# Performance work log

Measured on AMD Instinct MI355X. Metric: run time of the kernel, lower is better.

## Reference

```python
import jax, jax.numpy as jnp
import numpy as np

N, F, H, R, B, L, C, E, NB = 8192, 512, 256, 16, 32, 256, 7, 262144, 30
D = F + H


def setup_inputs() -> dict:
    ks = jax.random.split(jax.random.key(0), 16)
    g = lambda k, shape, fan: jax.random.normal(k, shape, jnp.float32) / np.sqrt(fan)
    return {
        "x": jax.random.normal(ks[0], (N, F), jnp.float32),
        "edge_index": jax.random.randint(ks[1], (2, E), 0, N),
        "edge_norm": jax.random.uniform(ks[2], (E,), jnp.float32),
        "edge_type": jax.random.randint(ks[3], (E,), 0, R),
        "seq_lengths": jnp.full((B,), L, dtype=jnp.int32),
        "umask": jnp.ones((B, L), jnp.float32),
        "nodal_attn": 1,
        "avec": 0,
        "basis": g(ks[4], (NB, F, H), F),
        "comp": g(ks[5], (R, NB), NB),
        "root1": g(ks[6], (F, H), F),
        "bias1": jnp.zeros((H,), jnp.float32),
        "w_rel": g(ks[7], (H, H), H),
        "b_rel": jnp.zeros((H,), jnp.float32),
        "w_root": g(ks[8], (H, H), H),
        "w_att": g(ks[9], (D, D), D),
        "b_att": jnp.zeros((D,), jnp.float32),
        "w_lin": g(ks[10], (D, H), D),
        "b_lin": jnp.zeros((H,), jnp.float32),
        "w_fc": g(ks[11], (H, C), H),
        "b_fc": jnp.zeros((C,), jnp.float32),
    }


def reference(x, edge_index, edge_norm, edge_type, seq_lengths, umask,
              nodal_attn, avec, basis, comp, root1, bias1, w_rel, b_rel,
              w_root, w_att, b_att, w_lin, b_lin, w_fc, b_fc):
    n = x.shape[0]
    r = comp.shape[0]
    src, dst = edge_index[0], edge_index[1]
    # ---- RGCNConv (num_bases basis decomposition, mean aggregation per relation, root + bias)
    W = jnp.einsum('rb,bfh->rfh', comp, basis)             # [R,F,H]
    xw = jnp.einsum('nf,rfh->nrh', x, W)                   # [N,R,H]
    msg = xw[src, edge_type]                               # [E,H] gather per edge
    seg = dst * r + edge_type                              # per (node, relation) segment
    cnt = jax.ops.segment_sum(jnp.ones((msg.shape[0],), msg.dtype), seg, num_segments=n * r)
    msg = msg / jnp.maximum(cnt[seg], 1.0)[:, None]
    out1 = jax.ops.segment_sum(msg, dst, num_segments=n) + x @ root1 + bias1
    # ---- GraphConv (add aggregation): W_rel * sum_j h_j + b_rel + W_root * h_i
    agg2 = jax.ops.segment_sum(out1[src], dst, num_segments=n)
    out2 = agg2 @ w_rel + b_rel + out1 @ w_root
    emotions = jnp.concatenate([x, out2], axis=-1)          # [N, F+H]
    if int(nodal_attn):
        seq = np.asarray(seq_lengths)                       # static conversation lengths
        starts = np.concatenate([[0], np.cumsum(seq)[:-1]])
        lmax = int(seq.max())
        rows = [jnp.pad(jax.lax.dynamic_slice_in_dim(emotions, int(s), int(l)),
                        ((0, lmax - int(l)), (0, 0)))
                for s, l in zip(starts, seq)]
        M = jnp.stack(rows, 0).transpose(1, 0, 2)           # [L, B, D]
        mask = umask                                        # [B, L]
        # MatchingAttention 'general2', vectorized over all timesteps t
        X = M @ w_att + b_att                               # transform(x_t) for every t: [L,B,D]
        Mm = M * mask.T[:, :, None]                         # mask memory over seq dim
        scores = jnp.einsum('tbd,sbd->tbs', X, Mm) * mask[None]
        a = jax.nn.softmax(jnp.tanh(scores), axis=-1) * mask[None]
        a = a / jnp.sum(a, axis=-1, keepdims=True)
        att = jnp.einsum('tbs,sbd->tbd', a, M)              # [L,B,D]
        hidden = jax.nn.relu(att @ w_lin + b_lin)
    else:
        hidden = jax.nn.relu(emotions @ w_lin + b_lin)
    # dropout is identity in eval mode
    logits = hidden @ w_fc + b_fc
    if int(avec):
        return logits
    return jax.nn.log_softmax(logits, axis=1)  # faithful: torch uses dim=1
```

## Files before the change

kernel.cpp:

```cpp
#include <hip/hip_runtime.h>
#include <hip/hip_bf16.h>

#define NN 8192
#define FF 512
#define HH 256
#define RR 16
#define BB 32
#define LL 256
#define CC 7
#define EE 262144
#define NBASE 30
#define DD 768

constexpr int FLAG_BIAS = 1, FLAG_RELU = 4, FLAG_TANH = 8,
              FLAG_SPLITOUT = 16, FLAG_TAILOUT = 32;

typedef __attribute__((ext_vector_type(8))) short bf16x8;
typedef __attribute__((ext_vector_type(4))) float f32x4;

__global__ __launch_bounds__(256) void detect_dtype(const unsigned short* __restrict__ xs,
                                                    int* __restrict__ flag) {
  __shared__ int red[256];
  int cnt = 0;
  for (int i = threadIdx.x * 2; i < 8192; i += 512) {
    unsigned short u = xs[i];
    int e = (u >> 7) & 0xFF;
    if (e >= 0xC0) cnt++;
  }
  red[threadIdx.x] = cnt;
  __syncthreads();
  for (int s = 128; s > 0; s >>= 1) {
    if (threadIdx.x < s) red[threadIdx.x] += red[threadIdx.x + s];
    __syncthreads();
  }
  if (threadIdx.x == 0) flag[0] = (red[0] > 16) ? 1 : 0;
}

struct ConvSeg {
  const void* src;
  float* dst;
  __hip_bfloat16* hi;
  __hip_bfloat16* lo;
  int n;
  int zero;
};
struct ConvTable {
  ConvSeg seg[12];
  int count;
  long total;
};

__global__ __launch_bounds__(256) void conv_all(ConvTable t, const int* __restrict__ flag) {
  const int fp32 = flag[0];
  for (long i = (long)blockIdx.x * 256 + threadIdx.x; i < t.total;
       i += (long)gridDim.x * 256) {
    long off = i;
    int s = 0;
    while (off >= t.seg[s].n) { off -= t.seg[s].n; s++; }
    const ConvSeg& sg = t.seg[s];
    float v = 0.f;
    if (!sg.zero)
      v = fp32 ? ((const float*)sg.src)[off]
               : __bfloat162float(((const __hip_bfloat16*)sg.src)[off]);
    if (sg.dst) sg.dst[off] = v;
    if (sg.hi) {
      __hip_bfloat16 h = __float2bfloat16(v);
      sg.hi[off] = h;
      sg.lo[off] = __float2bfloat16(v - __bfloat162float(h));
    }
  }
}

struct TSeg {
  const void* src;
  __hip_bfloat16* hi;
  __hip_bfloat16* lo;
  int R, C, ld, off;
};
struct TTable {
  TSeg seg[6];
  int count;
  long total;
};

__global__ __launch_bounds__(256) void split_t_all(TTable t, const int* __restrict__ flag) {
  const int fp32 = flag[0];
  for (long i = (long)blockIdx.x * 256 + threadIdx.x; i < t.total;
       i += (long)gridDim.x * 256) {
    long off = i;
    int s = 0;
    while (off >= (long)t.seg[s].R * t.seg[s].C) { off -= (long)t.seg[s].R * t.seg[s].C; s++; }
    const TSeg& sg = t.seg[s];
    int r = (int)(off % sg.R), c = (int)(off / sg.R);
    float v = fp32 ? ((const float*)sg.src)[(long)r * sg.C + c]
                   : __bfloat162float(((const __hip_bfloat16*)sg.src)[(long)r * sg.C + c]);
    __hip_bfloat16 h = __float2bfloat16(v);
    long d = (long)c * sg.ld + sg.off + r;
    sg.hi[d] = h;
    sg.lo[d] = __float2bfloat16(v - __bfloat162float(h));
  }
}

__global__ __launch_bounds__(256) void copy_xsplit(
    const __hip_bfloat16* __restrict__ xh, const __hip_bfloat16* __restrict__ xl,
    __hip_bfloat16* __restrict__ eh, __hip_bfloat16* __restrict__ el) {
  int idx = blockIdx.x * 256 + threadIdx.x;
  int n = idx >> 9, f = idx & 511;
  long d = (long)n * DD + f;
  eh[d] = xh[idx];
  el[d] = xl[idx];
}

__global__ __launch_bounds__(256) void transpose_emw(
    const __hip_bfloat16* __restrict__ hi_src, const __hip_bfloat16* __restrict__ lo_src,
    __hip_bfloat16* __restrict__ hi_dst, __hip_bfloat16* __restrict__ lo_dst) {
  __shared__ __hip_bfloat16 t[32][33];
  const int zz = blockIdx.z;
  const __hip_bfloat16* src = (zz < 32) ? hi_src : lo_src;
  __hip_bfloat16* dst = (zz < 32) ? hi_dst : lo_dst;
  const long b = zz & 31;
  const int d0 = blockIdx.x * 32, s0 = blockIdx.y * 32;
  const int c = threadIdx.x & 31, rw = threadIdx.x >> 5;
  const __hip_bfloat16* sp = src + b * (LL * 256);
  __hip_bfloat16* dp = dst + b * (LL * 256);
#pragma unroll
  for (int i = 0; i < 4; ++i)
    t[rw + i * 8][c] = sp[(long)(s0 + rw + i * 8) * 256 + d0 + c];
  __syncthreads();
#pragma unroll
  for (int i = 0; i < 4; ++i)
    dp[(long)(d0 + rw + i * 8) * 256 + s0 + c] = t[c][rw + i * 8];
}

__global__ __launch_bounds__(256) void wt_gemm(
    const float* __restrict__ basis, const float* __restrict__ comp,
    float* __restrict__ wt_nat) {
  __shared__ float cs[RR * NBASE];
  int tid = threadIdx.x;
  for (int i = tid; i < RR * NBASE; i += 256) cs[i] = comp[i];
  __syncthreads();
  long col = (long)blockIdx.x * 256 + tid;
  float acc[RR] = {};
  for (int b = 0; b < NBASE; ++b) {
    float v = basis[(long)b * 131072 + col];
#pragma unroll
    for (int r = 0; r < RR; ++r) acc[r] += cs[r * NBASE + b] * v;
  }
#pragma unroll
  for (int r = 0; r < RR; ++r) wt_nat[(long)r * 131072 + col] = acc[r];
}

__global__ __launch_bounds__(256) void wt_transpose(
    const float* __restrict__ wt_nat,
    __hip_bfloat16* __restrict__ hi, __hip_bfloat16* __restrict__ lo) {
  __shared__ float t[32][33];
  const int r = blockIdx.z;
  const int f0 = blockIdx.y * 32, h0 = blockIdx.x * 32;
  const int c = threadIdx.x & 31, rw = threadIdx.x >> 5;
  const float* src = wt_nat + ((long)r * 512 + f0) * 256 + h0;
#pragma unroll
  for (int i = 0; i < 4; ++i)
    t[rw + i * 8][c] = src[(long)(rw + i * 8) * 256 + c];
  __syncthreads();
#pragma unroll
  for (int i = 0; i < 4; ++i) {
    int hh = rw + i * 8;
    float v = t[c][hh];
    long orow = (long)(r * 256 + h0 + hh) * 512 + f0 + c;
    __hip_bfloat16 hv = __float2bfloat16(v);
    hi[orow] = hv;
    lo[orow] = __float2bfloat16(v - __bfloat162float(hv));
  }
}

__device__ __forceinline__ void gload_lds16(const void* g, void* l) {
  __builtin_amdgcn_global_load_lds(
      (const __attribute__((address_space(1))) unsigned int*)g,
      (__attribute__((address_space(3))) unsigned int*)l, 16, 0, 0);
}

__global__ __launch_bounds__(256, 3) void mfma_dual(
    const __hip_bfloat16* __restrict__ A, const __hip_bfloat16* __restrict__ Alo,
    const __hip_bfloat16* __restrict__ Bt, const __hip_bfloat16* __restrict__ Btlo,
    const float* __restrict__ bias, float* __restrict__ C, float* __restrict__ Ct,
    __hip_bfloat16* __restrict__ Chi, __hip_bfloat16* __restrict__ Clo,
    int K, int ldc, long sA, long sB, long sC, int flags) {
  __shared__ __hip_bfloat16 Ah[128 * 32];
  __shared__ __hip_bfloat16 Bh[128 * 32];
  __shared__ __hip_bfloat16 Al[128 * 32];
  __shared__ __hip_bfloat16 Bl[128 * 32];
  const int tid = threadIdx.x;
  const int w = tid >> 6, lane = tid & 63;
  const long z = blockIdx.z;
  const long row0 = (long)blockIdx.y * 128, col0 = (long)blockIdx.x * 128;
  const int wm = w & 1, wn = w >> 1;
  const int srow0 = (w * 128 + lane) >> 2;
  const int srow1 = (w * 128 + 64 + lane) >> 2;
  const int kch = (lane & 3) * 8;
  const int fr = lane & 15, q = lane >> 4;
  const bool hasAlo = (Alo != nullptr);
  const __hip_bfloat16* Az = A + z * sA;
  const __hip_bfloat16* Alz = hasAlo ? (Alo + z * sA) : nullptr;
  const __hip_bfloat16* Bz = Bt + z * sB;
  const __hip_bfloat16* Blz = Btlo + z * sB;
  const long aoff0 = (row0 + srow0) * K + kch, aoff1 = (row0 + srow1) * K + kch;
  const long boff0 = (col0 + srow0) * K + kch, boff1 = (col0 + srow1) * K + kch;
  f32x4 acc[4][4] = {};
  for (int k0 = 0; k0 < K; k0 += 32) {
    gload_lds16(Az + aoff0 + k0, Ah + w * 1024);
    gload_lds16(Az + aoff1 + k0, Ah + w * 1024 + 512);
    gload_lds16(Bz + boff0 + k0, Bh + w * 1024);
    gload_lds16(Bz + boff1 + k0, Bh + w * 1024 + 512);
    gload_lds16(Blz + boff0 + k0, Bl + w * 1024);
    gload_lds16(Blz + boff1 + k0, Bl + w * 1024 + 512);
    if (hasAlo) {
      gload_lds16(Alz + aoff0 + k0, Al + w * 1024);
      gload_lds16(Alz + aoff1 + k0, Al + w * 1024 + 512);
    }
    __syncthreads();
    bf16x8 ah[4], bh[4], bl[4];
#pragma unroll
    for (int i = 0; i < 4; ++i) {
      ah[i] = *(const bf16x8*)&Ah[(wm * 64 + i * 16 + fr) * 32 + q * 8];
      bh[i] = *(const bf16x8*)&Bh[(wn * 64 + i * 16 + fr) * 32 + q * 8];
      bl[i] = *(const bf16x8*)&Bl[(wn * 64 + i * 16 + fr) * 32 + q * 8];
    }
#pragma unroll
    for (int i = 0; i < 4; ++i)
#pragma unroll
      for (int j = 0; j < 4; ++j) {
        acc[i][j] = __builtin_amdgcn_mfma_f32_16x16x32_bf16(ah[i], bh[j], acc[i][j], 0, 0, 0);
        acc[i][j] = __builtin_amdgcn_mfma_f32_16x16x32_bf16(ah[i], bl[j], acc[i][j], 0, 0, 0);
      }
    if (hasAlo) {
      bf16x8 al[4];
#pragma unroll
      for (int i = 0; i < 4; ++i)
        al[i] = *(const bf16x8*)&Al[(wm * 64 + i * 16 + fr) * 32 + q * 8];
#pragma unroll
      for (int i = 0; i < 4; ++i)
#pragma unroll
        for (int j = 0; j < 4; ++j)
          acc[i][j] = __builtin_amdgcn_mfma_f32_16x16x32_bf16(al[i], bh[j], acc[i][j], 0, 0, 0);
    }
    __syncthreads();
  }
  const int cr = (lane >> 4) * 4, cc = lane & 15;
  float* Cz = C ? (C + z * sC) : nullptr;
  __hip_bfloat16* Chz = Chi ? (Chi + z * sC) : nullptr;
  __hip_bfloat16* Clz = Clo ? (Clo + z * sC) : nullptr;
#pragma unroll
  for (int i = 0; i < 4; ++i) {
    long rbase = row0 + wm * 64 + i * 16 + cr;
#pragma unroll
    for (int j = 0; j < 4; ++j) {
      long col = col0 + wn * 64 + j * 16 + cc;
      float bv = (flags & FLAG_BIAS) ? bias[col] : 0.f;
#pragma unroll
      for (int r = 0; r < 4; ++r) {
        float v = acc[i][j][r] + bv;
        if (flags & FLAG_RELU) v = fmaxf(v, 0.f);
        if (flags & FLAG_TANH) v = tanhf(v);
        if (flags & FLAG_SPLITOUT) {
          long off = (rbase + r) * ldc + col;
          __hip_bfloat16 hv = __float2bfloat16(v);
          Chz[off] = hv;
          Clz[off] = __float2bfloat16(v - __bfloat162float(hv));
        } else if ((flags & FLAG_TAILOUT) && col >= 4096) {
          Ct[(rbase + r) * 256 + (col - 4096)] = v;
        } else {
          Cz[(rbase + r) * ldc + col] = v;
        }
      }
    }
  }
}

__global__ __launch_bounds__(256) void count_edges(
    const int* __restrict__ ei, const int* __restrict__ et, float* __restrict__ cnt) {
  int e = blockIdx.x * 256 + threadIdx.x;
  if (e < EE) atomicAdd(&cnt[ei[EE + e] * RR + et[e]], 1.0f);
}

__global__ __launch_bounds__(256) void scan_rowptr(
    const float* __restrict__ cntf, int* __restrict__ rowptr, int* __restrict__ fill) {
  __shared__ int part[256];
  int tid = threadIdx.x;
  int base = tid * 32;
  int local[32];
  int s = 0;
  for (int i = 0; i < 32; ++i) {
    local[i] = s;
    const float* c = &cntf[(base + i) * RR];
    int d = 0;
#pragma unroll
    for (int r = 0; r < RR; ++r) d += (int)c[r];
    s += d;
  }
  part[tid] = s;
  __syncthreads();
  for (int off = 1; off < 256; off <<= 1) {
    int v = (tid >= off) ? part[tid - off] : 0;
    __syncthreads();
    part[tid] += v;
    __syncthreads();
  }
  int prev = (tid == 0) ? 0 : part[tid - 1];
  for (int i = 0; i < 32; ++i) rowptr[base + i] = prev + local[i];
  if (tid == 255) rowptr[8192] = part[255];
  for (int i = tid; i < 8192; i += 256) fill[i] = 0;
}

__global__ __launch_bounds__(256) void edge_fill(
    const int* __restrict__ ei, const int* __restrict__ et,
    const int* __restrict__ rowptr, int* __restrict__ fill, int* __restrict__ eidx) {
  int e = blockIdx.x * 256 + threadIdx.x;
  if (e < EE) {
    int dst = ei[EE + e];
    int pos = rowptr[dst] + atomicAdd(&fill[dst], 1);
    eidx[pos] = ei[e] | (et[e] << 16);
  }
}

__global__ __launch_bounds__(256) void rgcn_gather(
    const int* __restrict__ rowptr, const int* __restrict__ eidx,
    const float* __restrict__ cntf, const float* __restrict__ xw,
    float* __restrict__ out1, __hip_bfloat16* __restrict__ a2o1_hi,
    __hip_bfloat16* __restrict__ a2o1_lo) {
  const int dst = blockIdx.x;
  const int h = threadIdx.x;
  __shared__ float inv[RR];
  __shared__ int se[256];
  if (h < RR) inv[h] = 1.0f / fmaxf(cntf[dst * RR + h], 1.0f);
  const int beg = rowptr[dst], end = rowptr[dst + 1];
  float acc = 0.f;
  for (int c0 = beg; c0 < end; c0 += 256) {
    int n = min(256, end - c0);
    __syncthreads();
    if (h < n) se[h] = eidx[c0 + h];
    __syncthreads();
    for (int i = 0; i < n; ++i) {
      int pk = se[i];
      int src = pk & 0xFFFF, r = pk >> 16;
      acc += xw[((long)src << 12) + (r << 8) + h] * inv[r];
    }
  }
  float tot = out1[((long)dst << 8) + h] + acc;
  out1[((long)dst << 8) + h] = tot;
  __hip_bfloat16 hv = __float2bfloat16(tot);
  long d = (long)dst * 512 + 256 + h;
  a2o1_hi[d] = hv;
  a2o1_lo[d] = __float2bfloat16(tot - __bfloat162float(hv));
}

__global__ __launch_bounds__(256) void graphconv_gather(
    const int* __restrict__ rowptr, const int* __restrict__ eidx,
    const float* __restrict__ out1, __hip_bfloat16* __restrict__ a2o1_hi,
    __hip_bfloat16* __restrict__ a2o1_lo) {
  const int dst = blockIdx.x;
  const int h = threadIdx.x;
  __shared__ int se[256];
  const int beg = rowptr[dst], end = rowptr[dst + 1];
  float acc = 0.f;
  for (int c0 = beg; c0 < end; c0 += 256) {
    int n = min(256, end - c0);
    __syncthreads();
    if (h < n) se[h] = eidx[c0 + h];
    __syncthreads();
    for (int i = 0; i < n; ++i)
      acc += out1[((long)(se[i] & 0xFFFF) << 8) + h];
  }
  __hip_bfloat16 hv = __float2bfloat16(acc);
  long d = (long)dst * 512 + h;
  a2o1_hi[d] = hv;
  a2o1_lo[d] = __float2bfloat16(acc - __bfloat162float(hv));
}

__global__ __launch_bounds__(256) void softmax256(const float* __restrict__ S,
                                                  __hip_bfloat16* __restrict__ Ab) {
  __shared__ float red[256];
  long row = blockIdx.x;
  const float* p = S + row * 256;
  int t = threadIdx.x;
  float v = p[t];
  red[t] = v;
  __syncthreads();
  for (int s = 128; s > 0; s >>= 1) {
    if (t < s) red[t] = fmaxf(red[t], red[t + s]);
    __syncthreads();
  }
  float m = red[0];
  __syncthreads();
  float e = __expf(v - m);
  red[t] = e;
  __syncthreads();
  for (int s = 128; s > 0; s >>= 1) {
    if (t < s) red[t] += red[t + s];
    __syncthreads();
  }
  Ab[row * 256 + t] = __float2bfloat16(e / red[0]);
}

__global__ __launch_bounds__(256) void logits_lsm(
    const float* __restrict__ hidden, const float* __restrict__ w_fc,
    const float* __restrict__ b_fc, void* __restrict__ out_v,
    const int* __restrict__ flag) {
  __shared__ float wf[256 * 7];
  __shared__ float lg[224];
  __shared__ float corr[7];
  int t = blockIdx.x;
  int tid = threadIdx.x;
  for (int i = tid; i < 256 * 7; i += 256) wf[i] = w_fc[i];
  __syncthreads();
  if (tid < 224) {
    int b = tid / 7, c = tid % 7;
    const float* hr = hidden + ((long)((b << 8) + t) << 8);
    float s = b_fc[c];
    for (int k = 0; k < 256; ++k) s += hr[k] * wf[k * 7 + c];
    lg[tid] = s;
  }
  __syncthreads();
  if (tid < 7) {
    float m = -1e30f;
    for (int b = 0; b < BB; ++b) m = fmaxf(m, lg[b * 7 + tid]);
    float sum = 0.f;
    for (int b = 0; b < BB; ++b) sum += __expf(lg[b * 7 + tid] - m);
    corr[tid] = m + logf(sum);
  }
  __syncthreads();
  if (tid < 224) {
    float v = lg[tid] - corr[tid % 7];
    if (flag[0]) ((float*)out_v)[t * 224 + tid] = v;
    else ((__hip_bfloat16*)out_v)[t * 224 + tid] = __float2bfloat16(v);
  }
}

extern "C" void kernel_launch(void* const* d_in, const int* in_sizes, int n_in,
                              void* d_out, int out_size, void* d_ws, size_t ws_size,
                              hipStream_t stream) {
  const int* ei = (const int*)d_in[1];
  const int* et = (const int*)d_in[3];

  float* ws = (float*)d_ws;
  int* flag = (int*)d_ws;
  float* p = ws + 16;
  auto alloc = [&](long nf) { float* r = p; p += nf; return r; };
  float* w_fc_f = alloc(1792);
  float* b_rel_f = alloc(256);
  float* biasx = alloc(4352);
  float* b_att_f = alloc(768);
  float* b_lin_f = alloc(256);
  float* b_fc_f = alloc(16);
  __hip_bfloat16* wlin_hi = (__hip_bfloat16*)alloc(98304);
  __hip_bfloat16* wlin_lo = (__hip_bfloat16*)alloc(98304);
  __hip_bfloat16* x_hi = (__hip_bfloat16*)alloc(2097152);
  __hip_bfloat16* x_lo = (__hip_bfloat16*)alloc(2097152);
  __hip_bfloat16* watt_hi = (__hip_bfloat16*)alloc(294912);
  __hip_bfloat16* watt_lo = (__hip_bfloat16*)alloc(294912);
  __hip_bfloat16* wrr_hi = (__hip_bfloat16*)alloc(65536);
  __hip_bfloat16* wrr_lo = (__hip_bfloat16*)alloc(65536);
  __hip_bfloat16* wtc_hi = (__hip_bfloat16*)alloc(1114112);
  __hip_bfloat16* wtc_lo = (__hip_bfloat16*)alloc(1114112);
  float* basis_f = alloc(3932160);
  float* comp_f = alloc(512);
  float* xw = alloc(33554432);
  float* cnt = alloc(131072);
  float* out1 = alloc(2097152);
  __hip_bfloat16* a2o1_hi = (__hip_bfloat16*)alloc(2097152);
  __hip_bfloat16* a2o1_lo = (__hip_bfloat16*)alloc(2097152);
  float* hidden = alloc(2097152);
  int* rowptr = (int*)alloc(8208);
  int* fillc = (int*)alloc(8192);
  int* eidx = (int*)alloc(262144);
  float* wt_nat = xw;
  float* em = xw;
  __hip_bfloat16* emw_hi = (__hip_bfloat16*)em;
  __hip_bfloat16* emw_lo = (__hip_bfloat16*)(em + 1048576);
  __hip_bfloat16* emwT_hi = (__hip_bfloat16*)(em + 2097152);
  __hip_bfloat16* emwT_lo = (__hip_bfloat16*)(em + 3145728);
  __hip_bfloat16* em_hi = (__hip_bfloat16*)(em + 6291456);
  __hip_bfloat16* em_lo = (__hip_bfloat16*)(em + 9437184);
  __hip_bfloat16* X_hi = (__hip_bfloat16*)(em + 12582912);
  __hip_bfloat16* X_lo = (__hip_bfloat16*)(em + 15728640);
  float* scores = em + 18874368;
  __hip_bfloat16* a_b16 = (__hip_bfloat16*)(em + 20971520);

  detect_dtype<<<1, 256, 0, stream>>>((const unsigned short*)d_in[0], flag);
  ConvTable T{};
  long tot = 0;
  int ns = 0;
  auto seg = [&](const void* s, float* d, __hip_bfloat16* hi, __hip_bfloat16* lo,
                 int n, int z) {
    T.seg[ns].src = s; T.seg[ns].dst = d; T.seg[ns].hi = hi; T.seg[ns].lo = lo;
    T.seg[ns].n = n; T.seg[ns].zero = z; ns++; tot += n;
  };
  seg(d_in[0], nullptr, x_hi, x_lo, NN * FF, 0);
  seg(d_in[8], basis_f, nullptr, nullptr, NBASE * FF * HH, 0);
  seg(d_in[9], comp_f, nullptr, nullptr, RR * NBASE, 0);
  seg(d_in[13], b_rel_f, nullptr, nullptr, HH, 0);
  seg(d_in[16], b_att_f, nullptr, nullptr, DD, 0);
  seg(d_in[18], b_lin_f, nullptr, nullptr, HH, 0);
  seg(d_in[19], w_fc_f, nullptr, nullptr, HH * CC, 0);
  seg(d_in[20], b_fc_f, nullptr, nullptr, CC, 0);
  seg(nullptr, biasx, nullptr, nullptr, 4096, 1);
  seg(d_in[11], biasx + 4096, nullptr, nullptr, HH, 0);
  T.count = ns;
  T.total = tot;
  conv_all<<<4096, 256, 0, stream>>>(T, flag);
  TTable TT{};
  long ttot = 0;
  int ts = 0;
  auto tseg = [&](const void* s, __hip_bfloat16* hi, __hip_bfloat16* lo,
                  int R, int C, int ld, int off) {
    TT.seg[ts].src = s; TT.seg[ts].hi = hi; TT.seg[ts].lo = lo;
    TT.seg[ts].R = R; TT.seg[ts].C = C; TT.seg[ts].ld = ld; TT.seg[ts].off = off;
    ts++; ttot += (long)R * C;
  };
  tseg(d_in[15], watt_hi, watt_lo, DD, DD, DD, 0);
  tseg(d_in[17], wlin_hi, wlin_lo, DD, HH, DD, 0);
  tseg(d_in[10], wtc_hi + 4096 * 512, wtc_lo + 4096 * 512, FF, HH, FF, 0);
  tseg(d_in[12], wrr_hi, wrr_lo, HH, HH, 512, 0);
  tseg(d_in[14], wrr_hi, wrr_lo, HH, HH, 512, 256);
  TT.count = ts;
  TT.total = ttot;
  split_t_all<<<2048, 256, 0, stream>>>(TT, flag);

  wt_gemm<<<131072 / 256, 256, 0, stream>>>(basis_f, comp_f, wt_nat);
  wt_transpose<<<dim3(8, 16, 16), 256, 0, stream>>>(wt_nat, wtc_hi, wtc_lo);
  mfma_dual<<<dim3(34, 64, 1), 256, 0, stream>>>(
      x_hi, x_lo, wtc_hi, wtc_lo, biasx, xw, out1, nullptr, nullptr, FF, 4096,
      0, 0, 0, FLAG_BIAS | FLAG_TAILOUT);
  hipMemsetAsync(cnt, 0, 131072 * sizeof(float), stream);
  count_edges<<<EE / 256, 256, 0, stream>>>(ei, et, cnt);
  scan_rowptr<<<1, 256, 0, stream>>>(cnt, rowptr, fillc);
  edge_fill<<<EE / 256, 256, 0, stream>>>(ei, et, rowptr, fillc, eidx);
  rgcn_gather<<<NN, 256, 0, stream>>>(rowptr, eidx, cnt, xw, out1, a2o1_hi, a2o1_lo);
  graphconv_gather<<<NN, 256, 0, stream>>>(rowptr, eidx, out1, a2o1_hi, a2o1_lo);
  copy_xsplit<<<(NN * FF) / 256, 256, 0, stream>>>(x_hi, x_lo, em_hi, em_lo);
  mfma_dual<<<dim3(2, 64, 1), 256, 0, stream>>>(
      a2o1_hi, a2o1_lo, wrr_hi, wrr_lo, b_rel_f, nullptr, nullptr,
      em_hi + 512, em_lo + 512, 512, DD, 0, 0, 0, FLAG_BIAS | FLAG_SPLITOUT);
  mfma_dual<<<dim3(2, 64, 1), 256, 0, stream>>>(
      em_hi, em_lo, wlin_hi, wlin_lo, nullptr, nullptr, nullptr, emw_hi, emw_lo,
      DD, HH, 0, 0, 0, FLAG_SPLITOUT);
  transpose_emw<<<dim3(8, 8, 64), 256, 0, stream>>>(emw_hi, emw_lo, emwT_hi, emwT_lo);
  mfma_dual<<<dim3(6, 64, 1), 256, 0, stream>>>(
      em_hi, em_lo, watt_hi, watt_lo, b_att_f, nullptr, nullptr, X_hi, X_lo, DD, DD,
      0, 0, 0, FLAG_BIAS | FLAG_SPLITOUT);
  mfma_dual<<<dim3(2, 2, BB), 256, 0, stream>>>(
      X_hi, X_lo, em_hi, em_lo, nullptr, scores, nullptr, nullptr, nullptr, DD, LL,
      (long)LL * DD, (long)LL * DD, (long)LL * LL, FLAG_TANH);
  softmax256<<<BB * LL, 256, 0, stream>>>(scores, a_b16);
  mfma_dual<<<dim3(2, 2, BB), 256, 0, stream>>>(
      a_b16, nullptr, emwT_hi, emwT_lo, b_lin_f, hidden, nullptr, nullptr, nullptr,
      LL, HH, (long)LL * LL, (long)LL * HH, (long)LL * HH, FLAG_BIAS | FLAG_RELU);
  logits_lsm<<<LL, 256, 0, stream>>>(hidden, w_fc_f, b_fc_f, d_out, flag);
}
```

Measured before the change: 634.3 us.

## Merge prep kernels, fuse attention and linear GEMMs with transposed tail output

Merges the conversion and transposed-split prep kernels into one table-driven kernel. Concatenates w_att and w_lin into a single weight so one GEMM yields both X and em@w_lin. The w_lin columns are written directly in transposed per-batch layout, which removes a separate GEMM launch and the transpose kernel. Also unrolls the edge-gather loops into four independent accumulators to expose more memory-level parallelism. Adds dead scaffolding and an oddly declared copy kernel, and the unused hi2/lo2 path in the prep kernel risks confusion.

```diff
diff --git a/kernel.cpp b/kernel.cpp
--- a/kernel.cpp
+++ b/kernel.cpp
@@ -13,7 +13,7 @@
 #define DD 768
 
 constexpr int FLAG_BIAS = 1, FLAG_RELU = 4, FLAG_TANH = 8,
-              FLAG_SPLITOUT = 16, FLAG_TAILOUT = 32;
+              FLAG_SPLITOUT = 16, FLAG_TAILOUT = 32, FLAG_TAIL2 = 64;
 
 typedef __attribute__((ext_vector_type(8))) short bf16x8;
 typedef __attribute__((ext_vector_type(4))) float f32x4;
@@ -36,100 +36,59 @@
   if (threadIdx.x == 0) flag[0] = (red[0] > 16) ? 1 : 0;
 }
 
-struct ConvSeg {
+struct PSeg {
   const void* src;
   float* dst;
   __hip_bfloat16* hi;
   __hip_bfloat16* lo;
-  int n;
+  __hip_bfloat16* hi2;
+  __hip_bfloat16* lo2;
+  long n;
+  int R, C, ld, off;
+  int type;
   int zero;
 };
-struct ConvTable {
-  ConvSeg seg[12];
+struct PTable {
+  PSeg seg[16];
   int count;
   long total;
 };
 
-__global__ __launch_bounds__(256) void conv_all(ConvTable t, const int* __restrict__ flag) {
+__global__ __launch_bounds__(256) void prep_all(PTable t, const int* __restrict__ flag) {
   const int fp32 = flag[0];
   for (long i = (long)blockIdx.x * 256 + threadIdx.x; i < t.total;
        i += (long)gridDim.x * 256) {
     long off = i;
     int s = 0;
     while (off >= t.seg[s].n) { off -= t.seg[s].n; s++; }
-    const ConvSeg& sg = t.seg[s];
-    float v = 0.f;
-    if (!sg.zero)
-      v = fp32 ? ((const float*)sg.src)[off]
-               : __bfloat162float(((const __hip_bfloat16*)sg.src)[off]);
-    if (sg.dst) sg.dst[off] = v;
-    if (sg.hi) {
+    const PSeg& sg = t.seg[s];
+    if (sg.type == 0) {
+      float v = 0.f;
+      if (!sg.zero)
+        v = fp32 ? ((const float*)sg.src)[off]
+                 : __bfloat162float(((const __hip_bfloat16*)sg.src)[off]);
+      if (sg.dst) sg.dst[off] = v;
+      if (sg.hi) {
+        __hip_bfloat16 h = __float2bfloat16(v);
+        __hip_bfloat16 l = __float2bfloat16(v - __bfloat162float(h));
+        sg.hi[off] = h;
+        sg.lo[off] = l;
+        if (sg.hi2) {
+          long d2 = (off >> 9) * DD + (off & 511);
+          sg.hi2[d2] = h;
+          sg.lo2[d2] = l;
+        }
+      }
+    } else {
+      int r = (int)(off % sg.R), c = (int)(off / sg.R);
+      float v = fp32 ? ((const float*)sg.src)[(long)r * sg.C + c]
+                     : __bfloat162float(((const __hip_bfloat16*)sg.src)[(long)r * sg.C + c]);
       __hip_bfloat16 h = __float2bfloat16(v);
-      sg.hi[off] = h;
-      sg.lo[off] = __float2bfloat16(v - __bfloat162float(h));
-    }
-  }
-}
-
-struct TSeg {
-  const void* src;
-  __hip_bfloat16* hi;
-  __hip_bfloat16* lo;
-  int R, C, ld, off;
-};
-struct TTable {
-  TSeg seg[6];
-  int count;
-  long total;
-};
-
-__global__ __launch_bounds__(256) void split_t_all(TTable t, const int* __restrict__ flag) {
-  const int fp32 = flag[0];
-  for (long i = (long)blockIdx.x * 256 + threadIdx.x; i < t.total;
-       i += (long)gridDim.x * 256) {
-    long off = i;
-    int s = 0;
-    while (off >= (long)t.seg[s].R * t.seg[s].C) { off -= (long)t.seg[s].R * t.seg[s].C; s++; }
-    const TSeg& sg = t.seg[s];
-    int r = (int)(off % sg.R), c = (int)(off / sg.R);
-    float v = fp32 ? ((const float*)sg.src)[(long)r * sg.C + c]
-                   : __bfloat162float(((const __hip_bfloat16*)sg.src)[(long)r * sg.C + c]);
-    __hip_bfloat16 h = __float2bfloat16(v);
-    long d = (long)c * sg.ld + sg.off + r;
-    sg.hi[d] = h;
-    sg.lo[d] = __float2bfloat16(v - __bfloat162float(h));
-  }
-}
-
-__global__ __launch_bounds__(256) void copy_xsplit(
-    const __hip_bfloat16* __restrict__ xh, const __hip_bfloat16* __restrict__ xl,
-    __hip_bfloat16* __restrict__ eh, __hip_bfloat16* __restrict__ el) {
-  int idx = blockIdx.x * 256 + threadIdx.x;
-  int n = idx >> 9, f = idx & 511;
-  long d = (long)n * DD + f;
-  eh[d] = xh[idx];
-  el[d] = xl[idx];
-}
-
-__global__ __launch_bounds__(256) void transpose_emw(
-    const __hip_bfloat16* __restrict__ hi_src, const __hip_bfloat16* __restrict__ lo_src,
-    __hip_bfloat16* __restrict__ hi_dst, __hip_bfloat16* __restrict__ lo_dst) {
-  __shared__ __hip_bfloat16 t[32][33];
-  const int zz = blockIdx.z;
-  const __hip_bfloat16* src = (zz < 32) ? hi_src : lo_src;
-  __hip_bfloat16* dst = (zz < 32) ? hi_dst : lo_dst;
-  const long b = zz & 31;
-  const int d0 = blockIdx.x * 32, s0 = blockIdx.y * 32;
-  const int c = threadIdx.x & 31, rw = threadIdx.x >> 5;
-  const __hip_bfloat16* sp = src + b * (LL * 256);
-  __hip_bfloat16* dp = dst + b * (LL * 256);
-#pragma unroll
-  for (int i = 0; i < 4; ++i)
-    t[rw + i * 8][c] = sp[(long)(s0 + rw + i * 8) * 256 + d0 + c];
-  __syncthreads();
-#pragma unroll
-  for (int i = 0; i < 4; ++i)
-    dp[(long)(d0 + rw + i * 8) * 256 + s0 + c] = t[c][rw + i * 8];
+      long d = (long)c * sg.ld + sg.off + r;
+      sg.hi[d] = h;
+      sg.lo[d] = __float2bfloat16(v - __bfloat162float(h));
+    }
+  }
 }
 
 __global__ __launch_bounds__(256) void wt_gemm(
@@ -184,6 +143,7 @@
     const __hip_bfloat16* __restrict__ Bt, const __hip_bfloat16* __restrict__ Btlo,
     const float* __restrict__ bias, float* __restrict__ C, float* __restrict__ Ct,
     __hip_bfloat16* __restrict__ Chi, __hip_bfloat16* __restrict__ Clo,
+    __hip_bfloat16* __restrict__ Chi2, __hip_bfloat16* __restrict__ Clo2,
     int K, int ldc, long sA, long sB, long sC, int flags) {
   __shared__ __hip_bfloat16 Ah[128 * 32];
   __shared__ __hip_bfloat16 Bh[128 * 32];
@@ -261,15 +221,21 @@
         float v = acc[i][j][r] + bv;
         if (flags & FLAG_RELU) v = fmaxf(v, 0.f);
         if (flags & FLAG_TANH) v = tanhf(v);
-        if (flags & FLAG_SPLITOUT) {
-          long off = (rbase + r) * ldc + col;
+        long row = rbase + r;
+        if ((flags & FLAG_TAIL2) && col >= 768) {
+          long off2 = (row >> 8) * 65536 + (col - 768) * 256 + (row & 255);
+          __hip_bfloat16 hv = __float2bfloat16(v);
+          Chi2[off2] = hv;
+          Clo2[off2] = __float2bfloat16(v - __bfloat162float(hv));
+        } else if (flags & FLAG_SPLITOUT) {
+          long off = row * ldc + col;
           __hip_bfloat16 hv = __float2bfloat16(v);
           Chz[off] = hv;
           Clz[off] = __float2bfloat16(v - __bfloat162float(hv));
         } else if ((flags & FLAG_TAILOUT) && col >= 4096) {
-          Ct[(rbase + r) * 256 + (col - 4096)] = v;
+          Ct[row * 256 + (col - 4096)] = v;
         } else {
-          Cz[(rbase + r) * ldc + col] = v;
+          Cz[row * ldc + col] = v;
         }
       }
     }
@@ -333,19 +299,30 @@
   __shared__ int se[256];
   if (h < RR) inv[h] = 1.0f / fmaxf(cntf[dst * RR + h], 1.0f);
   const int beg = rowptr[dst], end = rowptr[dst + 1];
-  float acc = 0.f;
+  float a0 = 0.f, a1 = 0.f, a2 = 0.f, a3 = 0.f;
   for (int c0 = beg; c0 < end; c0 += 256) {
     int n = min(256, end - c0);
     __syncthreads();
     if (h < n) se[h] = eidx[c0 + h];
     __syncthreads();
-    for (int i = 0; i < n; ++i) {
+    int i = 0;
+    for (; i + 4 <= n; i += 4) {
+      int p0 = se[i], p1 = se[i + 1], p2 = se[i + 2], p3 = se[i + 3];
+      float v0 = xw[((long)(p0 & 0xFFFF) << 12) + ((p0 >> 16) << 8) + h];
+      float v1 = xw[((long)(p1 & 0xFFFF) << 12) + ((p1 >> 16) << 8) + h];
+      float v2 = xw[((long)(p2 & 0xFFFF) << 12) + ((p2 >> 16) << 8) + h];
+      float v3 = xw[((long)(p3 & 0xFFFF) << 12) + ((p3 >> 16) << 8) + h];
+      a0 += v0 * inv[p0 >> 16];
+      a1 += v1 * inv[p1 >> 16];
+      a2 += v2 * inv[p2 >> 16];
+      a3 += v3 * inv[p3 >> 16];
+    }
+    for (; i < n; ++i) {
       int pk = se[i];
-      int src = pk & 0xFFFF, r = pk >> 16;
-      acc += xw[((long)src << 12) + (r << 8) + h] * inv[r];
-    }
-  }
-  float tot = out1[((long)dst << 8) + h] + acc;
+      a0 += xw[((long)(pk & 0xFFFF) << 12) + ((pk >> 16) << 8) + h] * inv[pk >> 16];
+    }
+  }
+  float tot = out1[((long)dst << 8) + h] + ((a0 + a1) + (a2 + a3));
   out1[((long)dst << 8) + h] = tot;
   __hip_bfloat16 hv = __float2bfloat16(tot);
   long d = (long)dst * 512 + 256 + h;
@@ -361,15 +338,22 @@
   const int h = threadIdx.x;
   __shared__ int se[256];
   const int beg = rowptr[dst], end = rowptr[dst + 1];
-  float acc = 0.f;
+  float a0 = 0.f, a1 = 0.f, a2 = 0.f, a3 = 0.f;
   for (int c0 = beg; c0 < end; c0 += 256) {
     int n = min(256, end - c0);
     __syncthreads();
     if (h < n) se[h] = eidx[c0 + h];
     __syncthreads();
-    for (int i = 0; i < n; ++i)
-      acc += out1[((long)(se[i] & 0xFFFF) << 8) + h];
-  }
+    int i = 0;
+    for (; i + 4 <= n; i += 4) {
+      a0 += out1[((long)(se[i] & 0xFFFF) << 8) + h];
+      a1 += out1[((long)(se[i + 1] & 0xFFFF) << 8) + h];
+      a2 += out1[((long)(se[i + 2] & 0xFFFF) << 8) + h];
+      a3 += out1[((long)(se[i + 3] & 0xFFFF) << 8) + h];
+    }
+    for (; i < n; ++i) a0 += out1[((long)(se[i] & 0xFFFF) << 8) + h];
+  }
+  float acc = (a0 + a1) + (a2 + a3);
   __hip_bfloat16 hv = __float2bfloat16(acc);
   long d = (long)dst * 512 + h;
   a2o1_hi[d] = hv;
@@ -448,15 +432,13 @@
   float* w_fc_f = alloc(1792);
   float* b_rel_f = alloc(256);
   float* biasx = alloc(4352);
-  float* b_att_f = alloc(768);
+  float* battx = alloc(1024);
   float* b_lin_f = alloc(256);
   float* b_fc_f = alloc(16);
-  __hip_bfloat16* wlin_hi = (__hip_bfloat16*)alloc(98304);
-  __hip_bfloat16* wlin_lo = (__hip_bfloat16*)alloc(98304);
   __hip_bfloat16* x_hi = (__hip_bfloat16*)alloc(2097152);
   __hip_bfloat16* x_lo = (__hip_bfloat16*)alloc(2097152);
-  __hip_bfloat16* watt_hi = (__hip_bfloat16*)alloc(294912);
-  __hip_bfloat16* watt_lo = (__hip_bfloat16*)alloc(294912);
+  __hip_bfloat16* wae_hi = (__hip_bfloat16*)alloc(393216);
+  __hip_bfloat16* wae_lo = (__hip_bfloat16*)alloc(393216);
   __hip_bfloat16* wrr_hi = (__hip_bfloat16*)alloc(65536);
   __hip_bfloat16* wrr_lo = (__hip_bfloat16*)alloc(65536);
   __hip_bfloat16* wtc_hi = (__hip_bfloat16*)alloc(1114112);
@@ -474,8 +456,6 @@
   int* eidx = (int*)alloc(262144);
   float* wt_nat = xw;
   float* em = xw;
-  __hip_bfloat16* emw_hi = (__hip_bfloat16*)em;
-  __hip_bfloat16* emw_lo = (__hip_bfloat16*)(em + 1048576);
   __hip_bfloat16* emwT_hi = (__hip_bfloat16*)(em + 2097152);
   __hip_bfloat16* emwT_lo = (__hip_bfloat16*)(em + 3145728);
   __hip_bfloat16* em_hi = (__hip_bfloat16*)(em + 6291456);
@@ -486,73 +466,85 @@
   __hip_bfloat16* a_b16 = (__hip_bfloat16*)(em + 20971520);
 
   detect_dtype<<<1, 256, 0, stream>>>((const unsigned short*)d_in[0], flag);
-  ConvTable T{};
+  PTable T{};
   long tot = 0;
   int ns = 0;
-  auto seg = [&](const void* s, float* d, __hip_bfloat16* hi, __hip_bfloat16* lo,
-                 int n, int z) {
-    T.seg[ns].src = s; T.seg[ns].dst = d; T.seg[ns].hi = hi; T.seg[ns].lo = lo;
-    T.seg[ns].n = n; T.seg[ns].zero = z; ns++; tot += n;
+  auto segL = [&](const void* s, float* d, __hip_bfloat16* hi, __hip_bfloat16* lo,
+                  __hip_bfloat16* hi2, __hip_bfloat16* lo2, long n, int z) {
+    T.seg[ns] = PSeg{s, d, hi, lo, hi2, lo2, n, 0, 0, 0, 0, 0, z};
+    ns++; tot += n;
   };
-  seg(d_in[0], nullptr, x_hi, x_lo, NN * FF, 0);
-  seg(d_in[8], basis_f, nullptr, nullptr, NBASE * FF * HH, 0);
-  seg(d_in[9], comp_f, nullptr, nullptr, RR * NBASE, 0);
-  seg(d_in[13], b_rel_f, nullptr, nullptr, HH, 0);
-  seg(d_in[16], b_att_f, nullptr, nullptr, DD, 0);
-  seg(d_in[18], b_lin_f, nullptr, nullptr, HH, 0);
-  seg(d_in[19], w_fc_f, nullptr, nullptr, HH * CC, 0);
-  seg(d_in[20], b_fc_f, nullptr, nullptr, CC, 0);
-  seg(nullptr, biasx, nullptr, nullptr, 4096, 1);
-  seg(d_in[11], biasx + 4096, nullptr, nullptr, HH, 0);
+  auto segT = [&](const void* s, __hip_bfloat16* hi, __hip_bfloat16* lo,
+                  int R, int C, int ld, int off) {
+    T.seg[ns] = PSeg{s, nullptr, hi, lo, nullptr, nullptr, (long)R * C, R, C, ld, off, 1, 0};
+    ns++; tot += (long)R * C;
+  };
+  segL(d_in[0], nullptr, x_hi, x_lo, nullptr, nullptr, NN * FF, 0);
+  segL(d_in[8], basis_f, nullptr, nullptr, nullptr, nullptr, NBASE * FF * HH, 0);
+  segL(d_in[9], comp_f, nullptr, nullptr, nullptr, nullptr, RR * NBASE, 0);
+  segL(d_in[13], b_rel_f, nullptr, nullptr, nullptr, nullptr, HH, 0);
+  segL(d_in[16], battx, nullptr, nullptr, nullptr, nullptr, DD, 0);
+  segL(nullptr, battx + DD, nullptr, nullptr, nullptr, nullptr, 256, 1);
+  segL(d_in[18], b_lin_f, nullptr, nullptr, nullptr, nullptr, HH, 0);
+  segL(d_in[19], w_fc_f, nullptr, nullptr, nullptr, nullptr, HH * CC, 0);
+  segL(d_in[20], b_fc_f, nullptr, nullptr, nullptr, nullptr, CC, 0);
+  segL(nullptr, biasx, nullptr, nullptr, nullptr, nullptr, 4096, 1);
+  segL(d_in[11], biasx + 4096, nullptr, nullptr, nullptr, nullptr, HH, 0);
+  segT(d_in[15], wae_hi, wae_lo, DD, DD, DD, 0);
+  segT(d_in[17], wae_hi + 768 * 768, wae_lo + 768 * 768, DD, HH, DD, 0);
+  segT(d_in[10], wtc_hi + 4096 * 512, wtc_lo + 4096 * 512, FF, HH, FF, 0);
+  segT(d_in[12], wrr_hi, wrr_lo, HH, HH, 512, 0);
+  segT(d_in[14], wrr_hi, wrr_lo, HH, HH, 512, 256);
   T.count = ns;
   T.total = tot;
-  conv_all<<<4096, 256, 0, stream>>>(T, flag);
-  TTable TT{};
-  long ttot = 0;
-  int ts = 0;
-  auto tseg = [&](const void* s, __hip_bfloat16* hi, __hip_bfloat16* lo,
-                  int R, int C, int ld, int off) {
-    TT.seg[ts].src = s; TT.seg[ts].hi = hi; TT.seg[ts].lo = lo;
-    TT.seg[ts].R = R; TT.seg[ts].C = C; TT.seg[ts].ld = ld; TT.seg[ts].off = off;
-    ts++; ttot += (long)R * C;
-  };
-  tseg(d_in[15], watt_hi, watt_lo, DD, DD, DD, 0);
-  tseg(d_in[17], wlin_hi, wlin_lo, DD, HH, DD, 0);
-  tseg(d_in[10], wtc_hi + 4096 * 512, wtc_lo + 4096 * 512, FF, HH, FF, 0);
-  tseg(d_in[12], wrr_hi, wrr_lo, HH, HH, 512, 0);
-  tseg(d_in[14], wrr_hi, wrr_lo, HH, HH, 512, 256);
-  TT.count = ts;
-  TT.total = ttot;
-  split_t_all<<<2048, 256, 0, stream>>>(TT, flag);
+  prep_all<<<4096, 256, 0, stream>>>(T, flag);
 
   wt_gemm<<<131072 / 256, 256, 0, stream>>>(basis_f, comp_f, wt_nat);
   wt_transpose<<<dim3(8, 16, 16), 256, 0, stream>>>(wt_nat, wtc_hi, wtc_lo);
   mfma_dual<<<dim3(34, 64, 1), 256, 0, stream>>>(
-      x_hi, x_lo, wtc_hi, wtc_lo, biasx, xw, out1, nullptr, nullptr, FF, 4096,
-      0, 0, 0, FLAG_BIAS | FLAG_TAILOUT);
+      x_hi, x_lo, wtc_hi, wtc_lo, biasx, xw, out1, nullptr, nullptr, nullptr, nullptr,
+      FF, 4096, 0, 0, 0, FLAG_BIAS | FLAG_TAILOUT);
   hipMemsetAsync(cnt, 0, 131072 * sizeof(float), stream);
   count_edges<<<EE / 256, 256, 0, stream>>>(ei, et, cnt);
   scan_rowptr<<<1, 256, 0, stream>>>(cnt, rowptr, fillc);
   edge_fill<<<EE / 256, 256, 0, stream>>>(ei, et, rowptr, fillc, eidx);
   rgcn_gather<<<NN, 256, 0, stream>>>(rowptr, eidx, cnt, xw, out1, a2o1_hi, a2o1_lo);
   graphconv_gather<<<NN, 256, 0, stream>>>(rowptr, eidx, out1, a2o1_hi, a2o1_lo);
-  copy_xsplit<<<(NN * FF) / 256, 256, 0, stream>>>(x_hi, x_lo, em_hi, em_lo);
+  {
+    PTable T2{};
+    T2.seg[0] = PSeg{nullptr, nullptr, nullptr, nullptr, nullptr, nullptr,
+                     (long)NN * FF, 0, 0, 0, 0, 2, 0};
+  }
+  {
+    struct { const __hip_bfloat16 *xh, *xl; __hip_bfloat16 *eh, *el; } args{x_hi, x_lo, em_hi, em_lo};
+  }
+  extern __global__ void copy_xsplit_k(const __hip_bfloat16*, const __hip_bfloat16*,
+                                       __hip_bfloat16*, __hip_bfloat16*);
+  copy_xsplit_k<<<(NN * FF) / 256, 256, 0, stream>>>(x_hi, x_lo, em_hi, em_lo);
   mfma_dual<<<dim3(2, 64, 1), 256, 0, stream>>>(
       a2o1_hi, a2o1_lo, wrr_hi, wrr_lo, b_rel_f, nullptr, nullptr,
-      em_hi + 512, em_lo + 512, 512, DD, 0, 0, 0, FLAG_BIAS | FLAG_SPLITOUT);
-  mfma_dual<<<dim3(2, 64, 1), 256, 0, stream>>>(
-      em_hi, em_lo, wlin_hi, wlin_lo, nullptr, nullptr, nullptr, emw_hi, emw_lo,
-      DD, HH, 0, 0, 0, FLAG_SPLITOUT);
-  transpose_emw<<<dim3(8, 8, 64), 256, 0, stream>>>(emw_hi, emw_lo, emwT_hi, emwT_lo);
-  mfma_dual<<<dim3(6, 64, 1), 256, 0, stream>>>(
-      em_hi, em_lo, watt_hi, watt_lo, b_att_f, nullptr, nullptr, X_hi, X_lo, DD, DD,
-      0, 0, 0, FLAG_BIAS | FLAG_SPLITOUT);
+      em_hi + 512, em_lo + 512, nullptr, nullptr, 512, DD, 0, 0, 0,
+      FLAG_BIAS | FLAG_SPLITOUT);
+  mfma_dual<<<dim3(8, 64, 1), 256, 0, stream>>>(
+      em_hi, em_lo, wae_hi, wae_lo, battx, nullptr, nullptr, X_hi, X_lo,
+      emwT_hi, emwT_lo, DD, DD, 0, 0, 0, FLAG_BIAS | FLAG_SPLITOUT | FLAG_TAIL2);
   mfma_dual<<<dim3(2, 2, BB), 256, 0, stream>>>(
-      X_hi, X_lo, em_hi, em_lo, nullptr, scores, nullptr, nullptr, nullptr, DD, LL,
-      (long)LL * DD, (long)LL * DD, (long)LL * LL, FLAG_TANH);
+      X_hi, X_lo, em_hi, em_lo, nullptr, scores, nullptr, nullptr, nullptr,
+      nullptr, nullptr, DD, LL, (long)LL * DD, (long)LL * DD, (long)LL * LL, FLAG_TANH);
   softmax256<<<BB * LL, 256, 0, stream>>>(scores, a_b16);
   mfma_dual<<<dim3(2, 2, BB), 256, 0, stream>>>(
       a_b16, nullptr, emwT_hi, emwT_lo, b_lin_f, hidden, nullptr, nullptr, nullptr,
-      LL, HH, (long)LL * LL, (long)LL * HH, (long)LL * HH, FLAG_BIAS | FLAG_RELU);
+      nullptr, nullptr, LL, HH, (long)LL * LL, (long)LL * HH, (long)LL * HH,
+      FLAG_BIAS | FLAG_RELU);
   logits_lsm<<<LL, 256, 0, stream>>>(hidden, w_fc_f, b_fc_f, d_out, flag);
 }
+
+__global__ __launch_bounds__(256) void copy_xsplit_k(
+    const __hip_bfloat16* __restrict__ xh, const __hip_bfloat16* __restrict__ xl,
+    __hip_bfloat16* __restrict__ eh, __hip_bfloat16* __restrict__ el) {
+  int idx = blockIdx.x * 256 + threadIdx.x;
+  int n = idx >> 9, f = idx & 511;
+  long d = (long)n * DD + f;
+  eh[d] = xh[idx];
+  el[d] = xl[idx];
+}
```

Measured after the change: 622.7 us. No clear change (-1.8%).
